# Performance work log

Hardware: AMD Instinct MI355X
Metric: run time of the kernel (lower is better)

## Reference

```python
import jax, jax.numpy as jnp
import numpy as np

N, CIN, T = 10000, 64, 64
COUT, K = 64, 3


def setup_inputs() -> dict:
    key = jax.random.key(0)
    k1, k2, k3 = jax.random.split(key, 3)
    x = jax.random.normal(k1, (N, CIN, T), dtype=jnp.float32)
    # torch Conv1d default init: uniform(-1/sqrt(fan_in), 1/sqrt(fan_in))
    bound = 1.0 / np.sqrt(CIN * K)
    weight = jax.random.uniform(k2, (2 * COUT, CIN, K), dtype=jnp.float32, minval=-bound, maxval=bound)
    bias = jax.random.uniform(k3, (2 * COUT,), dtype=jnp.float32, minval=-bound, maxval=bound)
    return {"x": x, "weight": weight, "bias": bias}


def reference(x, weight, bias):
    # Batched 1D conv over time for all nodes at once (equivalent to the
    # per-node loop in the original, since weights are shared).
    # x: [N, Cin, T], weight: [2*Cout, Cin, K] -> y: [N, 2*Cout, T-K+1]
    y = jax.lax.conv_general_dilated(
        x, weight, window_strides=(1,), padding="VALID",
        dimension_numbers=("NCH", "OIH", "NCH"))
    y = y + bias[None, :, None]
    # GLU along channel dim: first half gated by sigmoid of second half
    a, b = jnp.split(y, 2, axis=1)
    return a * jax.nn.sigmoid(b)
```

## Files before the change

### kernel.cpp

```cpp
#include <hip/hip_runtime.h>
#include <hip/hip_bf16.h>

typedef __attribute__((ext_vector_type(8))) short short8;
typedef __attribute__((ext_vector_type(4))) float float4v;

#define NSAMP 10000
#define CIN   64
#define TLEN  64
#define COUT  64
#define TOUT  62

static __device__ __forceinline__ ushort f2bf(float v) {
    unsigned int x = __float_as_uint(v);
    return (ushort)((x + 0x7fffu + ((x >> 16) & 1u)) >> 16);
}

__global__ void prep_weights(const float* __restrict__ w, ushort* __restrict__ wa) {
    int o = blockIdx.x * blockDim.x + threadIdx.x;
    if (o >= 128 * 192) return;
    int co = o / 192;
    int kk = o - co * 192;
    int k  = kk >> 6;
    int ci = kk & 63;
    wa[o] = f2bf(w[co * 192 + ci * 3 + k]);
}

__global__ __launch_bounds__(256, 2)
void conv_glu(const float* __restrict__ x, const ushort* __restrict__ wa,
              const float* __restrict__ bias, float* __restrict__ out) {
    const int n   = blockIdx.x;
    const int tid = threadIdx.x;
    const int w   = tid >> 6;
    const int L   = tid & 63;
    const int l   = L & 15;
    const int q   = L >> 4;
    const int h   = w & 1;
    const int nh  = w >> 1;
    const int t0base = nh * 32;

    const float* xs = x + n * (CIN * TLEN);

    short8 afr[4][6];
#pragma unroll
    for (int mt = 0; mt < 4; ++mt) {
        int co = 32 * h + 16 * (mt & 1) + 64 * (mt >> 1) + l;
        const short8* wrow = (const short8*)(wa + co * 192);
#pragma unroll
        for (int kc = 0; kc < 6; ++kc)
            afr[mt][kc] = wrow[kc * 4 + q];
    }

    float4v acc[4][2];
#pragma unroll
    for (int mt = 0; mt < 4; ++mt)
#pragma unroll
        for (int nt = 0; nt < 2; ++nt)
            acc[mt][nt] = (float4v){0.f, 0.f, 0.f, 0.f};

#pragma unroll
    for (int kc = 0; kc < 6; ++kc) {
        const int kcv = kc >> 1;
        const int cib = (kc & 1) * 32 + q * 8;
#pragma unroll
        for (int nt = 0; nt < 2; ++nt) {
            int t = t0base + nt * 16 + l + kcv;
            if (t > 63) t = 63;
            const float* p = xs + cib * TLEN + t;
            short8 bfr;
#pragma unroll
            for (int j = 0; j < 8; ++j)
                bfr[j] = (short)f2bf(p[j * TLEN]);
#pragma unroll
            for (int mt = 0; mt < 4; ++mt)
                acc[mt][nt] = __builtin_amdgcn_mfma_f32_16x16x32_bf16(
                    afr[mt][kc], bfr, acc[mt][nt], 0, 0, 0);
        }
    }

#pragma unroll
    for (int p2 = 0; p2 < 2; ++p2) {
#pragma unroll
        for (int nt = 0; nt < 2; ++nt) {
#pragma unroll
            for (int r = 0; r < 4; ++r) {
                int co = 32 * h + 16 * p2 + 4 * q + r;
                int t  = t0base + nt * 16 + l;
                float a = acc[p2][nt][r]     + bias[co];
                float g = acc[p2 + 2][nt][r] + bias[co + 64];
                float sg = 1.0f / (1.0f + __expf(-g));
                if (t < TOUT)
                    out[(n * COUT + co) * TOUT + t] = a * sg;
            }
        }
    }
}

extern "C" void kernel_launch(void* const* d_in, const int* in_sizes, int n_in,
                              void* d_out, int out_size, void* d_ws, size_t ws_size,
                              hipStream_t stream) {
    const float* x    = (const float*)d_in[0];
    const float* wt   = (const float*)d_in[1];
    const float* bias = (const float*)d_in[2];
    ushort*      wa   = (ushort*)d_ws;
    float*       out  = (float*)d_out;

    prep_weights<<<96, 256, 0, stream>>>(wt, wa);
    conv_glu<<<NSAMP, 256, 0, stream>>>(x, wa, bias, out);
}
```

Measured before the change: 403.2 us.

## Stage bf16-converted input in LDS and repartition waves over time tiles

Each block now loads its sample's input once with coalesced float4 reads, converts it to bf16, and stores it in a padded shared-memory tile. MFMA B-fragments are then gathered from LDS instead of through strided scalar global loads that reconverted each value several times. Waves are split by time tile, with each wave computing all 8 output-channel tiles, so weight fragments are reloaded from global/L2 inside the loop rather than held in registers. Launch bounds are raised to 4 blocks per SM for more occupancy, at the cost of a barrier and extra weight-load traffic.

```diff
diff --git a/kernel.cpp b/kernel.cpp
--- a/kernel.cpp
+++ b/kernel.cpp
@@ -1,14 +1,9 @@
 #include <hip/hip_runtime.h>
-#include <hip/hip_bf16.h>
 
 typedef __attribute__((ext_vector_type(8))) short short8;
 typedef __attribute__((ext_vector_type(4))) float float4v;
 
 #define NSAMP 10000
-#define CIN   64
-#define TLEN  64
-#define COUT  64
-#define TOUT  62
 
 static __device__ __forceinline__ ushort f2bf(float v) {
     unsigned int x = __float_as_uint(v);
@@ -25,72 +20,63 @@
     wa[o] = f2bf(w[co * 192 + ci * 3 + k]);
 }
 
-__global__ __launch_bounds__(256, 2)
+__global__ __launch_bounds__(256, 4)
 void conv_glu(const float* __restrict__ x, const ushort* __restrict__ wa,
               const float* __restrict__ bias, float* __restrict__ out) {
+    __shared__ uint xt32[64 * 33];
+    const ushort* xt = (const ushort*)xt32;
+
     const int n   = blockIdx.x;
     const int tid = threadIdx.x;
     const int w   = tid >> 6;
     const int L   = tid & 63;
     const int l   = L & 15;
     const int q   = L >> 4;
-    const int h   = w & 1;
-    const int nh  = w >> 1;
-    const int t0base = nh * 32;
 
-    const float* xs = x + n * (CIN * TLEN);
+    const float4v* xg = (const float4v*)(x + n * 4096);
+#pragma unroll
+    for (int it = 0; it < 4; ++it) {
+        int ci = (tid >> 4) + 16 * it;
+        int tt = tid & 15;
+        float4v v = xg[ci * 16 + tt];
+        xt32[ci * 33 + tt * 2]     = (uint)f2bf(v.x) | ((uint)f2bf(v.y) << 16);
+        xt32[ci * 33 + tt * 2 + 1] = (uint)f2bf(v.z) | ((uint)f2bf(v.w) << 16);
+    }
+    __syncthreads();
 
-    short8 afr[4][6];
+    float4v acc[8];
 #pragma unroll
-    for (int mt = 0; mt < 4; ++mt) {
-        int co = 32 * h + 16 * (mt & 1) + 64 * (mt >> 1) + l;
-        const short8* wrow = (const short8*)(wa + co * 192);
-#pragma unroll
-        for (int kc = 0; kc < 6; ++kc)
-            afr[mt][kc] = wrow[kc * 4 + q];
-    }
+    for (int mt = 0; mt < 8; ++mt) acc[mt] = (float4v){0.f, 0.f, 0.f, 0.f};
 
-    float4v acc[4][2];
-#pragma unroll
-    for (int mt = 0; mt < 4; ++mt)
-#pragma unroll
-        for (int nt = 0; nt < 2; ++nt)
-            acc[mt][nt] = (float4v){0.f, 0.f, 0.f, 0.f};
+    const int t0 = 16 * w;
 
 #pragma unroll
     for (int kc = 0; kc < 6; ++kc) {
-        const int kcv = kc >> 1;
         const int cib = (kc & 1) * 32 + q * 8;
+        int t = t0 + l + (kc >> 1);
+        if (t > 63) t = 63;
+        short8 bfr;
 #pragma unroll
-        for (int nt = 0; nt < 2; ++nt) {
-            int t = t0base + nt * 16 + l + kcv;
-            if (t > 63) t = 63;
-            const float* p = xs + cib * TLEN + t;
-            short8 bfr;
+        for (int j = 0; j < 8; ++j)
+            bfr[j] = (short)xt[(cib + j) * 66 + t];
 #pragma unroll
-            for (int j = 0; j < 8; ++j)
-                bfr[j] = (short)f2bf(p[j * TLEN]);
-#pragma unroll
-            for (int mt = 0; mt < 4; ++mt)
-                acc[mt][nt] = __builtin_amdgcn_mfma_f32_16x16x32_bf16(
-                    afr[mt][kc], bfr, acc[mt][nt], 0, 0, 0);
+        for (int mt = 0; mt < 8; ++mt) {
+            short8 afr = *(const short8*)(wa + (mt * 16 + l) * 192 + kc * 32 + q * 8);
+            acc[mt] = __builtin_amdgcn_mfma_f32_16x16x32_bf16(afr, bfr, acc[mt], 0, 0, 0);
         }
     }
 
+    const int t = t0 + l;
 #pragma unroll
-    for (int p2 = 0; p2 < 2; ++p2) {
+    for (int p2 = 0; p2 < 4; ++p2) {
 #pragma unroll
-        for (int nt = 0; nt < 2; ++nt) {
-#pragma unroll
-            for (int r = 0; r < 4; ++r) {
-                int co = 32 * h + 16 * p2 + 4 * q + r;
-                int t  = t0base + nt * 16 + l;
-                float a = acc[p2][nt][r]     + bias[co];
-                float g = acc[p2 + 2][nt][r] + bias[co + 64];
-                float sg = 1.0f / (1.0f + __expf(-g));
-                if (t < TOUT)
-                    out[(n * COUT + co) * TOUT + t] = a * sg;
-            }
+        for (int r = 0; r < 4; ++r) {
+            int co = p2 * 16 + q * 4 + r;
+            float a = acc[p2][r]     + bias[co];
+            float g = acc[p2 + 4][r] + bias[co + 64];
+            float sg = 1.0f / (1.0f + __expf(-g));
+            if (t < 62)
+                out[(n * 64 + co) * 62 + t] = a * sg;
         }
     }
 }
```

Result: slower. 454.3 us (+12.7%).
